# Performance work log

Hardware: AMD Instinct MI355X
Metric: run time of the kernel (lower is better)

## Reference

```python
import jax, jax.numpy as jnp
import numpy as np

DIM = 512
H = 8
D = 64
EPS = 1e-5


def _ln(x, g, b):
    m = jnp.mean(x, axis=-1, keepdims=True)
    v = jnp.var(x, axis=-1, keepdims=True)
    return (x - m) * jax.lax.rsqrt(v + EPS) * g + b


def _attn(x, ctx, wq, wk, wv, wo, bo):
    B, S, _ = x.shape
    T = ctx.shape[1]
    q = (x @ wq).reshape(B, S, H, D)
    k = (ctx @ wk).reshape(B, T, H, D)
    v = (ctx @ wv).reshape(B, T, H, D)
    scale = D ** -0.5
    score = jnp.einsum('bqhd,bkhd->bhqk', q, k) * scale  # [B,H,S,T]
    w = jax.nn.softmax(score, axis=-1)
    o = jnp.einsum('bhqk,bkhd->bqhd', w, v).reshape(B, S, H * D)
    return o @ wo + bo


def _geglu(x, w, b):
    h = x @ w + b
    y, gate = h[..., :4 * DIM], h[..., 4 * DIM:]
    tanh_res = jnp.tanh(gate * 0.7978845608 * (1.0 + 0.044715 * gate * gate))
    return y * 0.5 * gate * (1.0 + tanh_res)


def setup_inputs() -> dict:
    key = jax.random.key(0)
    ks = jax.random.split(key, 16)
    s = 0.02
    inp = {
        'x': jax.random.normal(ks[0], (2, 4096, DIM), jnp.float32),
        'context': jax.random.normal(ks[1], (2, 77, DIM), jnp.float32),
        'ln1_g': jnp.ones((DIM,), jnp.float32),
        'ln1_b': jnp.zeros((DIM,), jnp.float32),
        'wq1': jax.random.normal(ks[2], (DIM, H * D), jnp.float32) * s,
        'wk1': jax.random.normal(ks[3], (DIM, H * D), jnp.float32) * s,
        'wv1': jax.random.normal(ks[4], (DIM, H * D), jnp.float32) * s,
        'wo1': jax.random.normal(ks[5], (H * D, H * D), jnp.float32) * s,
        'bo1': jnp.zeros((H * D,), jnp.float32),
        'ln2_g': jnp.ones((DIM,), jnp.float32),
        'ln2_b': jnp.zeros((DIM,), jnp.float32),
        'wq2': jax.random.normal(ks[6], (DIM, H * D), jnp.float32) * s,
        'wk2': jax.random.normal(ks[7], (DIM, H * D), jnp.float32) * s,
        'wv2': jax.random.normal(ks[8], (DIM, H * D), jnp.float32) * s,
        'wo2': jax.random.normal(ks[9], (H * D, H * D), jnp.float32) * s,
        'bo2': jnp.zeros((H * D,), jnp.float32),
        'ln3_g': jnp.ones((DIM,), jnp.float32),
        'ln3_b': jnp.zeros((DIM,), jnp.float32),
        'geglu_w': jax.random.normal(ks[10], (DIM, 8 * DIM), jnp.float32) * s,
        'geglu_b': jnp.zeros((8 * DIM,), jnp.float32),
        'out_w': jax.random.normal(ks[11], (4 * DIM, DIM), jnp.float32) * s,
        'out_b': jnp.zeros((DIM,), jnp.float32),
    }
    return inp


def reference(x, context, ln1_g, ln1_b, wq1, wk1, wv1, wo1, bo1,
              ln2_g, ln2_b, wq2, wk2, wv2, wo2, bo2,
              ln3_g, ln3_b, geglu_w, geglu_b, out_w, out_b):
    h = _attn(_ln(x, ln1_g, ln1_b), _ln(x, ln1_g, ln1_b), wq1, wk1, wv1, wo1, bo1) + x
    h = _attn(_ln(h, ln2_g, ln2_b), context, wq2, wk2, wv2, wo2, bo2) + h
    ff = _geglu(_ln(h, ln3_g, ln3_b), geglu_w, geglu_b)
    return ff @ out_w + out_b + h
```

## Files before the change

kernel.cpp:

```cpp
#include <hip/hip_runtime.h>
#include <hip/hip_bf16.h>
#include <math.h>

#define DIM 512
#define NHEAD 8
#define HD 64
#define BATCH 2
#define SEQ 4096
#define CTXLEN 77
#define NTOK (BATCH*SEQ)
#define NCTX (BATCH*CTXLEN)

typedef __hip_bfloat16 bf16;
typedef __attribute__((ext_vector_type(8))) short bf8_t;
typedef __attribute__((ext_vector_type(4))) float f4_t;

__device__ __forceinline__ float b2f(bf16 v){ return __bfloat162float(v); }
__device__ __forceinline__ bf16  f2b(float v){ return __float2bfloat16(v); }
__device__ __forceinline__ unsigned int packbf2(float a, float b){
    unsigned int au = __float_as_uint(a) + 0x8000u;
    unsigned int bu = __float_as_uint(b) + 0x8000u;
    return __builtin_amdgcn_perm(bu, au, 0x07060302u);
}
__device__ __forceinline__ void  stf(float* p, float v){ *p = v; }
__device__ __forceinline__ void  stf(bf16* p, float v){ *p = f2b(v); }

__device__ __forceinline__ void glds16(const bf16* g, unsigned short* l){
    __builtin_amdgcn_global_load_lds(
        (__attribute__((address_space(1))) void*)g,
        (__attribute__((address_space(3))) void*)l,
        16, 0, 0);
}

__global__ __launch_bounds__(256)
void ln_kernel(const float* __restrict__ x, const float* __restrict__ g,
               const float* __restrict__ b, bf16* __restrict__ out, int nrows)
{
    int row  = blockIdx.x * 4 + (threadIdx.x >> 6);
    int lane = threadIdx.x & 63;
    if (row >= nrows) return;
    const float* xr = x + (size_t)row * DIM;
    float v[8];
    float s = 0.f, sq = 0.f;
    #pragma unroll
    for (int j = 0; j < 8; ++j) {
        float f = xr[lane + 64*j];
        v[j] = f; s += f; sq += f*f;
    }
    #pragma unroll
    for (int off = 32; off; off >>= 1) {
        s  += __shfl_xor(s,  off);
        sq += __shfl_xor(sq, off);
    }
    float mean = s * (1.f/DIM);
    float var  = sq * (1.f/DIM) - mean*mean;
    float rstd = rsqrtf(var + 1e-5f);
    bf16* orow = out + (size_t)row * DIM;
    #pragma unroll
    for (int j = 0; j < 8; ++j) {
        int c = lane + 64*j;
        orow[c] = f2b((v[j]-mean)*rstd*g[c] + b[c]);
    }
}

__global__ __launch_bounds__(256)
void transpose_bf16_kernel(const float* __restrict__ W, bf16* __restrict__ Wt, int K, int N)
{
    __shared__ float tile[32][33];
    int n0 = blockIdx.x * 32, k0 = blockIdx.y * 32;
    int tx = threadIdx.x & 31, ty = threadIdx.x >> 5;
    #pragma unroll
    for (int p = 0; p < 4; ++p)
        tile[ty + p*8][tx] = W[(size_t)(k0 + ty + p*8)*N + n0 + tx];
    __syncthreads();
    #pragma unroll
    for (int p = 0; p < 4; ++p)
        Wt[(size_t)(n0 + ty + p*8)*K + k0 + tx] = f2b(tile[tx][ty + p*8]);
}

struct TPtrs { const float* src[8]; bf16* dst[8]; };
__global__ __launch_bounds__(256)
void transpose8_kernel(TPtrs p)
{
    __shared__ float tile[32][33];
    const float* W = p.src[blockIdx.z];
    bf16* Wt = p.dst[blockIdx.z];
    int n0 = blockIdx.x * 32, k0 = blockIdx.y * 32;
    int tx = threadIdx.x & 31, ty = threadIdx.x >> 5;
    #pragma unroll
    for (int q = 0; q < 4; ++q)
        tile[ty + q*8][tx] = W[(size_t)(k0 + ty + q*8)*512 + n0 + tx];
    __syncthreads();
    #pragma unroll
    for (int q = 0; q < 4; ++q)
        Wt[(size_t)(n0 + ty + q*8)*512 + k0 + tx] = f2b(tile[tx][ty + q*8]);
}

__global__ __launch_bounds__(256)
void cast_bf16_kernel(const float* __restrict__ in, bf16* __restrict__ out, int n)
{
    int i = blockIdx.x*256 + threadIdx.x;
    if (i < n) out[i] = f2b(in[i]);
}

__global__ __launch_bounds__(256)
void v_transpose_kernel(const bf16* __restrict__ V, bf16* __restrict__ Vt, int T, int pitch)
{
    __shared__ __align__(16) unsigned short tile[64*64];
    const int tid = threadIdx.x;
    const int b = blockIdx.z, h = blockIdx.y;
    const int t0 = blockIdx.x * 64;
    #pragma unroll
    for (int it = 0; it < 2; ++it) {
        int e = tid + it*256;
        int t = e >> 3, c = e & 7;
        int gk = t0 + t;
        bf8_t v = {0,0,0,0,0,0,0,0};
        if (gk < T) v = *(const bf8_t*)(V + ((size_t)(b*T + gk))*DIM + h*HD + c*8);
        *(bf8_t*)&tile[t*64 + c*8] = v;
    }
    __syncthreads();
    #pragma unroll
    for (int it = 0; it < 2; ++it) {
        int e = tid + it*256;
        int d = e & 63, oc = e >> 6;
        unsigned short tmp[8];
        #pragma unroll
        for (int j = 0; j < 8; ++j) tmp[j] = tile[(oc*8 + j)*64 + d];
        *(bf8_t*)(Vt + ((size_t)((b*8 + h)*64 + d))*pitch + t0 + oc*8) = *(bf8_t*)tmp;
    }
}

struct OutPtrs { void* p[3]; };
template<int RESID, typename OUTT, bool GUARD>
__global__ __launch_bounds__(256)
void gemm_mfma_kernel(const bf16* __restrict__ A, const bf16* __restrict__ Wt,
                      const float* __restrict__ bias, const float* __restrict__ resid,
                      OutPtrs outs, int M, int K)
{
    __shared__ __align__(16) unsigned short As[2][128*64];
    __shared__ __align__(16) unsigned short Bs[2][64*64];
    const int tid  = threadIdx.x;
    const int wave = tid >> 6, lane = tid & 63;
    const int l16  = lane & 15, quad = lane >> 4;
    const int wm = (wave >> 1) * 64, wn = (wave & 1) * 32;
    const int m0 = blockIdx.y * 128, n0 = blockIdx.x * 64;
    OUTT* outp = (OUTT*)outs.p[n0 >> 9];
    const int lc0 = n0 & 511;
    const int lr = lane >> 3;
    const int lc = (lane & 7) ^ lr;

    f4_t acc[4][2];
    #pragma unroll
    for (int i = 0; i < 4; ++i) { acc[i][0] = f4_t{0,0,0,0}; acc[i][1] = f4_t{0,0,0,0}; }

    auto stage = [&](int k0, int bf) {
        #pragma unroll
        for (int i = 0; i < 4; ++i) {
            int r = (wave*4 + i)*8 + lr;
            int gr = m0 + r;
            if (GUARD) gr = (gr < M) ? gr : (M-1);
            glds16(A + (size_t)gr*K + k0 + lc*8, &As[bf][(wave*4 + i)*512]);
        }
        #pragma unroll
        for (int j = 0; j < 2; ++j) {
            int r = (wave*2 + j)*8 + lr;
            glds16(Wt + (size_t)(n0 + r)*K + k0 + lc*8, &Bs[bf][(wave*2 + j)*512]);
        }
    };

    stage(0, 0);
    __syncthreads();

    for (int k0 = 0; k0 < K; k0 += 64) {
        const int bf = (k0 >> 6) & 1;
        if (k0 + 64 < K) stage(k0 + 64, bf ^ 1);
        #pragma unroll
        for (int kc = 0; kc < 2; ++kc) {
            const int cg = kc*4 + quad;
            bf8_t af[4], bfr[2];
            #pragma unroll
            for (int mt = 0; mt < 4; ++mt) {
                int r = wm + mt*16 + l16;
                af[mt] = *(const bf8_t*)&As[bf][r*64 + ((cg ^ (r&7))*8)];
            }
            #pragma unroll
            for (int nt = 0; nt < 2; ++nt) {
                int r = wn + nt*16 + l16;
                bfr[nt] = *(const bf8_t*)&Bs[bf][r*64 + ((cg ^ (r&7))*8)];
            }
            #pragma unroll
            for (int mt = 0; mt < 4; ++mt)
                #pragma unroll
                for (int nt = 0; nt < 2; ++nt)
                    acc[mt][nt] = __builtin_amdgcn_mfma_f32_16x16x32_bf16(af[mt], bfr[nt], acc[mt][nt], 0, 0, 0);
        }
        __syncthreads();
    }

    #pragma unroll
    for (int mt = 0; mt < 4; ++mt) {
        #pragma unroll
        for (int r_ = 0; r_ < 4; ++r_) {
            int row = m0 + wm + mt*16 + quad*4 + r_;
            if (GUARD && row >= M) continue;
            size_t rb = (size_t)row * 512;
            #pragma unroll
            for (int nt = 0; nt < 2; ++nt) {
                int col = lc0 + wn + nt*16 + l16;
                float v = acc[mt][nt][r_];
                if (bias) v += bias[col];
                if (RESID) v += resid[rb + col];
                stf(&outp[rb + col], v);
            }
        }
    }
}

__global__ __launch_bounds__(256)
void geglu_mfma_kernel(const bf16* __restrict__ A, const bf16* __restrict__ WtG,
                       const float* __restrict__ bias, bf16* __restrict__ outp)
{
    __shared__ __align__(16) unsigned short As[128*64];
    __shared__ __align__(16) unsigned short Bys[64*64];
    __shared__ __align__(16) unsigned short Bgs[64*64];
    const int tid  = threadIdx.x;
    const int wave = tid >> 6, lane = tid & 63;
    const int l16  = lane & 15, quad = lane >> 4;
    const int m0 = blockIdx.y * 128, n0 = blockIdx.x * 64;
    const int lr = lane >> 3;
    const int lc = (lane & 7) ^ lr;

    f4_t accy[2][4], accg[2][4];
    #pragma unroll
    for (int i = 0; i < 2; ++i)
        #pragma unroll
        for (int j = 0; j < 4; ++j) { accy[i][j] = f4_t{0,0,0,0}; accg[i][j] = f4_t{0,0,0,0}; }

    for (int k0 = 0; k0 < DIM; k0 += 64) {
        #pragma unroll
        for (int i = 0; i < 4; ++i) {
            int r = (wave*4 + i)*8 + lr;
            glds16(A + (size_t)(m0 + r)*DIM + k0 + lc*8, &As[(wave*4 + i)*512]);
        }
        #pragma unroll
        for (int j = 0; j < 2; ++j) {
            int r = (wave*2 + j)*8 + lr;
            glds16(WtG + (size_t)(n0 + r)*DIM + k0 + lc*8, &Bys[(wave*2 + j)*512]);
            glds16(WtG + (size_t)(2048 + n0 + r)*DIM + k0 + lc*8, &Bgs[(wave*2 + j)*512]);
        }
        __syncthreads();
        #pragma unroll
        for (int kc = 0; kc < 2; ++kc) {
            const int cg = kc*4 + quad;
            bf8_t af[2];
            #pragma unroll
            for (int mt = 0; mt < 2; ++mt) {
                int r = wave*32 + mt*16 + l16;
                af[mt] = *(const bf8_t*)&As[r*64 + ((cg ^ (r&7))*8)];
            }
            #pragma unroll
            for (int nt = 0; nt < 4; ++nt) {
                int r = nt*16 + l16;
                bf8_t by = *(const bf8_t*)&Bys[r*64 + ((cg ^ (r&7))*8)];
                bf8_t bg = *(const bf8_t*)&Bgs[r*64 + ((cg ^ (r&7))*8)];
                #pragma unroll
                for (int mt = 0; mt < 2; ++mt) {
                    accy[mt][nt] = __builtin_amdgcn_mfma_f32_16x16x32_bf16(af[mt], by, accy[mt][nt], 0, 0, 0);
                    accg[mt][nt] = __builtin_amdgcn_mfma_f32_16x16x32_bf16(af[mt], bg, accg[mt][nt], 0, 0, 0);
                }
            }
        }
        __syncthreads();
    }

    #pragma unroll
    for (int mt = 0; mt < 2; ++mt) {
        #pragma unroll
        for (int r_ = 0; r_ < 4; ++r_) {
            int row = m0 + wave*32 + mt*16 + quad*4 + r_;
            size_t rb = (size_t)row * 2048;
            #pragma unroll
            for (int nt = 0; nt < 4; ++nt) {
                int col = n0 + nt*16 + l16;
                float y = accy[mt][nt][r_] + bias[col];
                float g = accg[mt][nt][r_] + bias[2048 + col];
                float t = tanhf(0.7978845608f*g*(1.f + 0.044715f*g*g));
                outp[rb + col] = f2b(y * 0.5f * g * (1.f + t));
            }
        }
    }
}

__global__ __launch_bounds__(512)
void attn_mfma_kernel(const bf16* __restrict__ Qm, const bf16* __restrict__ Km,
                      const bf16* __restrict__ VtG, bf16* __restrict__ Om,
                      int T, int vpitch)
{
    __shared__ __align__(16) unsigned short Ks[2][64*64];
    __shared__ __align__(16) unsigned short Vts[2][64*64];

    const int tid  = threadIdx.x;
    const int wave = tid >> 6, lane = tid & 63;
    const int l16  = lane & 15, quad = lane >> 4;
    const int b = blockIdx.z, h = blockIdx.y;
    const int qblk = blockIdx.x * 128;
    const int lr = lane >> 3;
    const int lc = (lane & 7) ^ lr;
    const int srow = wave*8 + lr;

    bf8_t ones;
    #pragma unroll
    for (int j = 0; j < 8; ++j) ((unsigned short*)&ones)[j] = 0x3F80;

    bf8_t qf[2];
    {
        const bf16* qp = Qm + ((size_t)(b*SEQ + qblk + wave*16 + l16))*DIM + h*HD + quad*8;
        #pragma unroll
        for (int kc = 0; kc < 2; ++kc) {
            bf8_t v = *(const bf8_t*)(qp + kc*32);
            unsigned short* u = (unsigned short*)&v;
            unsigned int* w = (unsigned int*)&v;
            #pragma unroll
            for (int j = 0; j < 4; ++j) {
                float f0 = b2f(*(bf16*)&u[2*j])   * 0.1803368801f;
                float f1 = b2f(*(bf16*)&u[2*j+1]) * 0.1803368801f;
                w[j] = packbf2(f0, f1);
            }
            qf[kc] = v;
        }
    }

    f4_t o[4];
    #pragma unroll
    for (int dt = 0; dt < 4; ++dt) o[dt] = f4_t{0,0,0,0};
    f4_t lacc = {0,0,0,0};

    const bf16* Kbase = Km + (size_t)b*T*DIM + h*HD;
    const bf16* Vbase = VtG + ((size_t)((b*8 + h)*64 + srow))*vpitch;

    {
        int gk = srow; if (gk > T-1) gk = T-1;
        glds16(Kbase + (size_t)gk*DIM + lc*8, &Ks[0][wave*512]);
        glds16(Vbase + lc*8,                  &Vts[0][wave*512]);
    }
    __syncthreads();

    const int ntiles = (T + 63) >> 6;
    for (int t0 = 0; t0 < ntiles; ++t0) {
        const int kb = t0 << 6;
        const int cur = t0 & 1;
        if (t0 + 1 < ntiles) {
            int gk = kb + 64 + srow; if (gk > T-1) gk = T-1;
            glds16(Kbase + (size_t)gk*DIM + lc*8,  &Ks[cur^1][wave*512]);
            glds16(Vbase + kb + 64 + lc*8,         &Vts[cur^1][wave*512]);
        }

        bf8_t kf[4][2], vf[4][2];
        #pragma unroll
        for (int t = 0; t < 4; ++t) {
            int r = t*16 + l16;
            #pragma unroll
            for (int kc = 0; kc < 2; ++kc) {
                int cg = kc*4 + quad;
                kf[t][kc] = *(const bf8_t*)&Ks[cur][r*64 + ((cg ^ (r&7))*8)];
                vf[t][kc] = *(const bf8_t*)&Vts[cur][r*64 + ((cg ^ (r&7))*8)];
            }
        }
        const bool tail = (kb + 64 > T);

        f4_t sc4[4];
        #pragma unroll
        for (int km = 0; km < 4; ++km) {
            f4_t c = {0,0,0,0};
            c = __builtin_amdgcn_mfma_f32_16x16x32_bf16(kf[km][0], qf[0], c, 0, 0, 0);
            c = __builtin_amdgcn_mfma_f32_16x16x32_bf16(kf[km][1], qf[1], c, 0, 0, 0);
            sc4[km] = c;
        }
        if (tail) {
            #pragma unroll
            for (int km = 0; km < 4; ++km)
                #pragma unroll
                for (int r = 0; r < 4; ++r)
                    if (kb + km*16 + quad*4 + r >= T) sc4[km][r] = -1e30f;
        }
        unsigned int pk[4][2];
        #pragma unroll
        for (int km = 0; km < 4; ++km) {
            pk[km][0] = packbf2(exp2f(sc4[km][0]), exp2f(sc4[km][1]));
            pk[km][1] = packbf2(exp2f(sc4[km][2]), exp2f(sc4[km][3]));
        }
        #pragma unroll
        for (int kc = 0; kc < 2; ++kc) {
            auto s0 = __builtin_amdgcn_permlane32_swap(pk[2*kc][0], pk[2*kc+1][0], false, false);
            auto w02 = __builtin_amdgcn_permlane16_swap(s0[0], s0[1], false, false);
            auto s1 = __builtin_amdgcn_permlane32_swap(pk[2*kc][1], pk[2*kc+1][1], false, false);
            auto w13 = __builtin_amdgcn_permlane16_swap(s1[0], s1[1], false, false);
            union { unsigned int u[4]; bf8_t v; } pfu;
            pfu.u[0] = w02[0]; pfu.u[1] = w13[0]; pfu.u[2] = w02[1]; pfu.u[3] = w13[1];
            bf8_t pf = pfu.v;
            lacc = __builtin_amdgcn_mfma_f32_16x16x32_bf16(ones, pf, lacc, 0, 0, 0);
            #pragma unroll
            for (int dt = 0; dt < 4; ++dt)
                o[dt] = __builtin_amdgcn_mfma_f32_16x16x32_bf16(vf[dt][kc], pf, o[dt], 0, 0, 0);
        }
        __syncthreads();
    }

    {
        float inv = 1.f / lacc[0];
        int tok = qblk + wave*16 + l16;
        size_t base = ((size_t)(b*SEQ + tok))*DIM + h*HD;
        #pragma unroll
        for (int dt = 0; dt < 4; ++dt) {
            uint2 w;
            w.x = packbf2(o[dt][0]*inv, o[dt][1]*inv);
            w.y = packbf2(o[dt][2]*inv, o[dt][3]*inv);
            *(uint2*)(Om + base + dt*16 + quad*4) = w;
        }
    }
}

extern "C" void kernel_launch(void* const* d_in, const int* in_sizes, int n_in,
                              void* d_out, int out_size, void* d_ws, size_t ws_size,
                              hipStream_t stream)
{
    (void)in_sizes; (void)n_in; (void)out_size; (void)ws_size;
    const float* x    = (const float*)d_in[0];
    const float* ctx  = (const float*)d_in[1];
    const float* ln1g = (const float*)d_in[2];
    const float* ln1b = (const float*)d_in[3];
    const float* wq1  = (const float*)d_in[4];
    const float* wk1  = (const float*)d_in[5];
    const float* wv1  = (const float*)d_in[6];
    const float* wo1  = (const float*)d_in[7];
    const float* bo1  = (const float*)d_in[8];
    const float* ln2g = (const float*)d_in[9];
    const float* ln2b = (const float*)d_in[10];
    const float* wq2  = (const float*)d_in[11];
    const float* wk2  = (const float*)d_in[12];
    const float* wv2  = (const float*)d_in[13];
    const float* wo2  = (const float*)d_in[14];
    const float* bo2  = (const float*)d_in[15];
    const float* ln3g = (const float*)d_in[16];
    const float* ln3b = (const float*)d_in[17];
    const float* gw   = (const float*)d_in[18];
    const float* gb   = (const float*)d_in[19];
    const float* ow   = (const float*)d_in[20];
    const float* ob   = (const float*)d_in[21];
    float* out = (float*)d_out;

    char* ws = (char*)d_ws;
    bf16* An  = (bf16*)(ws);
    bf16* VtG = (bf16*)(ws);
    bf16* Qb  = (bf16*)(ws + ((size_t)8<<20));
    bf16* Kb  = (bf16*)(ws + ((size_t)16<<20));
    bf16* Vb  = (bf16*)(ws + ((size_t)24<<20));
    bf16* Ob  = (bf16*)(ws + ((size_t)32<<20));
    bf16* FF  = Qb;
    float* Hf = out;
    bf16* WT  = (bf16*)(ws + ((size_t)40<<20));
    bf16* wq1T = WT + 0*262144, *wk1T = WT + 1*262144, *wv1T = WT + 2*262144, *wo1T = WT + 3*262144;
    bf16* wq2T = WT + 4*262144, *wk2T = WT + 5*262144, *wv2T = WT + 6*262144, *wo2T = WT + 7*262144;
    bf16* gwT  = (bf16*)(ws + ((size_t)44<<20));
    bf16* owT  = (bf16*)(ws + ((size_t)48<<20));
    bf16* ctxb = (bf16*)(ws + ((size_t)50<<20));
    bf16* VtG2 = (bf16*)(ws + ((size_t)50<<20) + ((size_t)512<<10));

    dim3 blk(256);
    dim3 blkA(512);

    TPtrs tp;
    tp.src[0]=wq1; tp.src[1]=wk1; tp.src[2]=wv1; tp.src[3]=wo1;
    tp.src[4]=wq2; tp.src[5]=wk2; tp.src[6]=wv2; tp.src[7]=wo2;
    tp.dst[0]=wq1T; tp.dst[1]=wk1T; tp.dst[2]=wv1T; tp.dst[3]=wo1T;
    tp.dst[4]=wq2T; tp.dst[5]=wk2T; tp.dst[6]=wv2T; tp.dst[7]=wo2T;
    transpose8_kernel<<<dim3(16,16,8), blk, 0, stream>>>(tp);
    transpose_bf16_kernel<<<dim3(128,16), blk, 0, stream>>>(gw, gwT, DIM, 4096);
    transpose_bf16_kernel<<<dim3(16,64), blk, 0, stream>>>(ow, owT, 2048, DIM);
    cast_bf16_kernel<<<dim3((NCTX*DIM+255)/256), blk, 0, stream>>>(ctx, ctxb, NCTX*DIM);

    dim3 gLN(NTOK/4);
    dim3 gQKV(24, 64);
    dim3 gG(8, 64);
    dim3 gKVx(16, 2);
    dim3 gGEGLU(32, 64);
    dim3 gATT(SEQ/128, NHEAD, BATCH);
    OutPtrs oQKV{{Qb, Kb, Vb}};
    OutPtrs oKVx{{Kb, Vb, nullptr}};
    OutPtrs oQ{{Qb, nullptr, nullptr}};
    OutPtrs oH{{Hf, nullptr, nullptr}};
    OutPtrs oOut{{out, nullptr, nullptr}};

    ln_kernel<<<gLN, blk, 0, stream>>>(x, ln1g, ln1b, An, NTOK);
    gemm_mfma_kernel<0,bf16,false><<<gQKV, blk, 0, stream>>>(An, wq1T, nullptr, nullptr, oQKV, NTOK, DIM);
    v_transpose_kernel<<<dim3(SEQ/64, NHEAD, BATCH), blk, 0, stream>>>(Vb, VtG, SEQ, SEQ);
    attn_mfma_kernel<<<gATT, blkA, 0, stream>>>(Qb, Kb, VtG, Ob, SEQ, SEQ);
    gemm_mfma_kernel<1,float,false><<<gG, blk, 0, stream>>>(Ob, wo1T, bo1, x, oH, NTOK, DIM);

    ln_kernel<<<gLN, blk, 0, stream>>>(Hf, ln2g, ln2b, An, NTOK);
    gemm_mfma_kernel<0,bf16,false><<<gG, blk, 0, stream>>>(An, wq2T, nullptr, nullptr, oQ, NTOK, DIM);
    gemm_mfma_kernel<0,bf16,true><<<gKVx, blk, 0, stream>>>(ctxb, wk2T, nullptr, nullptr, oKVx, NCTX, DIM);
    v_transpose_kernel<<<dim3(2, NHEAD, BATCH), blk, 0, stream>>>(Vb, VtG2, CTXLEN, 128);
    attn_mfma_kernel<<<gATT, blkA, 0, stream>>>(Qb, Kb, VtG2, Ob, CTXLEN, 128);
    gemm_mfma_kernel<1,float,false><<<gG, blk, 0, stream>>>(Ob, wo2T, bo2, Hf, oH, NTOK, DIM);

    ln_kernel<<<gLN, blk, 0, stream>>>(Hf, ln3g, ln3b, An, NTOK);
    geglu_mfma_kernel<<<gGEGLU, blk, 0, stream>>>(An, gwT, gb, FF);
    gemm_mfma_kernel<1,float,false><<<gG, blk, 0, stream>>>(FF, owT, ob, Hf, oOut, NTOK, 2048);
}
```

Before: 472.2 us.

## Add 128x128 GEMM tile kernel and restage attention K/V and P through LDS

Adds a 128x128-tile MFMA GEMM and uses it for the fused QKV projection and the FFN output projection. Larger tiles raise operand reuse but halve the block count, leaving only 256 blocks for the output GEMM. Separately, the attention kernel drops the double-buffered direct-to-LDS K/V loads for register-staged single-buffer stores with an extra barrier per tile. It also replaces the permlane swaps that reshuffle P with a write and read through a per-wave LDS scratch. This trades cross-lane permutes for extra LDS traffic and loses overlap between loads and compute.

```diff
diff --git a/kernel.cpp b/kernel.cpp
--- a/kernel.cpp
+++ b/kernel.cpp
@@ -132,6 +132,7 @@
 }
 
 struct OutPtrs { void* p[3]; };
+
 template<int RESID, typename OUTT, bool GUARD>
 __global__ __launch_bounds__(256)
 void gemm_mfma_kernel(const bf16* __restrict__ A, const bf16* __restrict__ Wt,
@@ -217,6 +218,93 @@
     }
 }
 
+template<int RESID, typename OUTT, bool GUARD>
+__global__ __launch_bounds__(256)
+void gemm128_kernel(const bf16* __restrict__ A, const bf16* __restrict__ Wt,
+                    const float* __restrict__ bias, const float* __restrict__ resid,
+                    OutPtrs outs, int M, int K)
+{
+    __shared__ __align__(16) unsigned short As[2][128*64];
+    __shared__ __align__(16) unsigned short Bs[2][128*64];
+    const int tid  = threadIdx.x;
+    const int wave = tid >> 6, lane = tid & 63;
+    const int l16  = lane & 15, quad = lane >> 4;
+    const int wm = (wave >> 1) * 64, wn = (wave & 1) * 64;
+    const int m0 = blockIdx.y * 128, n0 = blockIdx.x * 128;
+    OUTT* outp = (OUTT*)outs.p[n0 >> 9];
+    const int lc0 = n0 & 511;
+    const int lr = lane >> 3;
+    const int lc = (lane & 7) ^ lr;
+
+    f4_t acc[4][4];
+    #pragma unroll
+    for (int i = 0; i < 4; ++i)
+        #pragma unroll
+        for (int j = 0; j < 4; ++j) acc[i][j] = f4_t{0,0,0,0};
+
+    auto stage = [&](int k0, int bf) {
+        #pragma unroll
+        for (int i = 0; i < 4; ++i) {
+            int r = (wave*4 + i)*8 + lr;
+            int gr = m0 + r;
+            if (GUARD) gr = (gr < M) ? gr : (M-1);
+            glds16(A + (size_t)gr*K + k0 + lc*8, &As[bf][(wave*4 + i)*512]);
+        }
+        #pragma unroll
+        for (int i = 0; i < 4; ++i) {
+            int r = (wave*4 + i)*8 + lr;
+            glds16(Wt + (size_t)(n0 + r)*K + k0 + lc*8, &Bs[bf][(wave*4 + i)*512]);
+        }
+    };
+
+    stage(0, 0);
+    __syncthreads();
+
+    for (int k0 = 0; k0 < K; k0 += 64) {
+        const int bf = (k0 >> 6) & 1;
+        if (k0 + 64 < K) stage(k0 + 64, bf ^ 1);
+        #pragma unroll
+        for (int kc = 0; kc < 2; ++kc) {
+            const int cg = kc*4 + quad;
+            bf8_t af[4], bfr[4];
+            #pragma unroll
+            for (int mt = 0; mt < 4; ++mt) {
+                int r = wm + mt*16 + l16;
+                af[mt] = *(const bf8_t*)&As[bf][r*64 + ((cg ^ (r&7))*8)];
+            }
+            #pragma unroll
+            for (int nt = 0; nt < 4; ++nt) {
+                int r = wn + nt*16 + l16;
+                bfr[nt] = *(const bf8_t*)&Bs[bf][r*64 + ((cg ^ (r&7))*8)];
+            }
+            #pragma unroll
+            for (int mt = 0; mt < 4; ++mt)
+                #pragma unroll
+                for (int nt = 0; nt < 4; ++nt)
+                    acc[mt][nt] = __builtin_amdgcn_mfma_f32_16x16x32_bf16(af[mt], bfr[nt], acc[mt][nt], 0, 0, 0);
+        }
+        __syncthreads();
+    }
+
+    #pragma unroll
+    for (int mt = 0; mt < 4; ++mt) {
+        #pragma unroll
+        for (int r_ = 0; r_ < 4; ++r_) {
+            int row = m0 + wm + mt*16 + quad*4 + r_;
+            if (GUARD && row >= M) continue;
+            size_t rb = (size_t)row * 512;
+            #pragma unroll
+            for (int nt = 0; nt < 4; ++nt) {
+                int col = lc0 + wn + nt*16 + l16;
+                float v = acc[mt][nt][r_];
+                if (bias) v += bias[col];
+                if (RESID) v += resid[rb + col];
+                stf(&outp[rb + col], v);
+            }
+        }
+    }
+}
+
 __global__ __launch_bounds__(256)
 void geglu_mfma_kernel(const bf16* __restrict__ A, const bf16* __restrict__ WtG,
                        const float* __restrict__ bias, bf16* __restrict__ outp)
@@ -297,17 +385,16 @@
                       const bf16* __restrict__ VtG, bf16* __restrict__ Om,
                       int T, int vpitch)
 {
-    __shared__ __align__(16) unsigned short Ks[2][64*64];
-    __shared__ __align__(16) unsigned short Vts[2][64*64];
+    __shared__ __align__(16) unsigned short Ks[64*64];
+    __shared__ __align__(16) unsigned short Vts[64*64];
+    __shared__ __align__(16) unsigned short Ps[8][16*64];
 
     const int tid  = threadIdx.x;
     const int wave = tid >> 6, lane = tid & 63;
     const int l16  = lane & 15, quad = lane >> 4;
     const int b = blockIdx.z, h = blockIdx.y;
     const int qblk = blockIdx.x * 128;
-    const int lr = lane >> 3;
-    const int lc = (lane & 7) ^ lr;
-    const int srow = wave*8 + lr;
+    const int sr = tid >> 3, sc_ = tid & 7;
 
     bf8_t ones;
     #pragma unroll
@@ -337,23 +424,24 @@
     f4_t lacc = {0,0,0,0};
 
     const bf16* Kbase = Km + (size_t)b*T*DIM + h*HD;
-    const bf16* Vbase = VtG + ((size_t)((b*8 + h)*64 + srow))*vpitch;
-
-    {
-        int gk = srow; if (gk > T-1) gk = T-1;
-        glds16(Kbase + (size_t)gk*DIM + lc*8, &Ks[0][wave*512]);
-        glds16(Vbase + lc*8,                  &Vts[0][wave*512]);
-    }
-    __syncthreads();
+    const bf16* Vbase = VtG + ((size_t)((b*8 + h)*64 + sr))*vpitch;
+
+    bf8_t kq, vq;
+    kq = bf8_t{0,0,0,0,0,0,0,0};
+    if (sr < T) kq = *(const bf8_t*)(Kbase + (size_t)sr*DIM + sc_*8);
+    vq = *(const bf8_t*)(Vbase + sc_*8);
 
     const int ntiles = (T + 63) >> 6;
     for (int t0 = 0; t0 < ntiles; ++t0) {
         const int kb = t0 << 6;
-        const int cur = t0 & 1;
+        *(bf8_t*)&Ks[sr*64 + ((sc_ ^ (sr&7))*8)]  = kq;
+        *(bf8_t*)&Vts[sr*64 + ((sc_ ^ (sr&7))*8)] = vq;
+        __syncthreads();
         if (t0 + 1 < ntiles) {
-            int gk = kb + 64 + srow; if (gk > T-1) gk = T-1;
-            glds16(Kbase + (size_t)gk*DIM + lc*8,  &Ks[cur^1][wave*512]);
-            glds16(Vbase + kb + 64 + lc*8,         &Vts[cur^1][wave*512]);
+            int gk = kb + 64 + sr;
+            kq = bf8_t{0,0,0,0,0,0,0,0};
+            if (gk < T) kq = *(const bf8_t*)(Kbase + (size_t)gk*DIM + sc_*8);
+            vq = *(const bf8_t*)(Vbase + kb + 64 + sc_*8);
         }
 
         bf8_t kf[4][2], vf[4][2];
@@ -363,8 +451,8 @@
             #pragma unroll
             for (int kc = 0; kc < 2; ++kc) {
                 int cg = kc*4 + quad;
-                kf[t][kc] = *(const bf8_t*)&Ks[cur][r*64 + ((cg ^ (r&7))*8)];
-                vf[t][kc] = *(const bf8_t*)&Vts[cur][r*64 + ((cg ^ (r&7))*8)];
+                kf[t][kc] = *(const bf8_t*)&Ks[r*64 + ((cg ^ (r&7))*8)];
+                vf[t][kc] = *(const bf8_t*)&Vts[r*64 + ((cg ^ (r&7))*8)];
             }
         }
         const bool tail = (kb + 64 > T);
@@ -384,21 +472,19 @@
                 for (int r = 0; r < 4; ++r)
                     if (kb + km*16 + quad*4 + r >= T) sc4[km][r] = -1e30f;
         }
-        unsigned int pk[4][2];
         #pragma unroll
         for (int km = 0; km < 4; ++km) {
-            pk[km][0] = packbf2(exp2f(sc4[km][0]), exp2f(sc4[km][1]));
-            pk[km][1] = packbf2(exp2f(sc4[km][2]), exp2f(sc4[km][3]));
+            uint2 w;
+            w.x = packbf2(exp2f(sc4[km][0]), exp2f(sc4[km][1]));
+            w.y = packbf2(exp2f(sc4[km][2]), exp2f(sc4[km][3]));
+            int chunk = 2*km + (quad >> 1);
+            int a = l16*64 + ((chunk ^ (l16 & 7))*8) + (quad & 1)*4;
+            *(uint2*)&Ps[wave][a] = w;
         }
         #pragma unroll
         for (int kc = 0; kc < 2; ++kc) {
-            auto s0 = __builtin_amdgcn_permlane32_swap(pk[2*kc][0], pk[2*kc+1][0], false, false);
-            auto w02 = __builtin_amdgcn_permlane16_swap(s0[0], s0[1], false, false);
-            auto s1 = __builtin_amdgcn_permlane32_swap(pk[2*kc][1], pk[2*kc+1][1], false, false);
-            auto w13 = __builtin_amdgcn_permlane16_swap(s1[0], s1[1], false, false);
-            union { unsigned int u[4]; bf8_t v; } pfu;
-            pfu.u[0] = w02[0]; pfu.u[1] = w13[0]; pfu.u[2] = w02[1]; pfu.u[3] = w13[1];
-            bf8_t pf = pfu.v;
+            int cg = kc*4 + quad;
+            bf8_t pf = *(const bf8_t*)&Ps[wave][l16*64 + ((cg ^ (l16 & 7))*8)];
             lacc = __builtin_amdgcn_mfma_f32_16x16x32_bf16(ones, pf, lacc, 0, 0, 0);
             #pragma unroll
             for (int dt = 0; dt < 4; ++dt)
@@ -481,10 +567,11 @@
     cast_bf16_kernel<<<dim3((NCTX*DIM+255)/256), blk, 0, stream>>>(ctx, ctxb, NCTX*DIM);
 
     dim3 gLN(NTOK/4);
-    dim3 gQKV(24, 64);
+    dim3 gQKV(12, 64);
     dim3 gG(8, 64);
     dim3 gKVx(16, 2);
     dim3 gGEGLU(32, 64);
+    dim3 gOUT(4, 64);
     dim3 gATT(SEQ/128, NHEAD, BATCH);
     OutPtrs oQKV{{Qb, Kb, Vb}};
     OutPtrs oKVx{{Kb, Vb, nullptr}};
@@ -493,7 +580,7 @@
     OutPtrs oOut{{out, nullptr, nullptr}};
 
     ln_kernel<<<gLN, blk, 0, stream>>>(x, ln1g, ln1b, An, NTOK);
-    gemm_mfma_kernel<0,bf16,false><<<gQKV, blk, 0, stream>>>(An, wq1T, nullptr, nullptr, oQKV, NTOK, DIM);
+    gemm128_kernel<0,bf16,false><<<gQKV, blk, 0, stream>>>(An, wq1T, nullptr, nullptr, oQKV, NTOK, DIM);
     v_transpose_kernel<<<dim3(SEQ/64, NHEAD, BATCH), blk, 0, stream>>>(Vb, VtG, SEQ, SEQ);
     attn_mfma_kernel<<<gATT, blkA, 0, stream>>>(Qb, Kb, VtG, Ob, SEQ, SEQ);
     gemm_mfma_kernel<1,float,false><<<gG, blk, 0, stream>>>(Ob, wo1T, bo1, x, oH, NTOK, DIM);
@@ -507,5 +594,5 @@
 
     ln_kernel<<<gLN, blk, 0, stream>>>(Hf, ln3g, ln3b, An, NTOK);
     geglu_mfma_kernel<<<gGEGLU, blk, 0, stream>>>(An, gwT, gb, FF);
-    gemm_mfma_kernel<1,float,false><<<gG, blk, 0, stream>>>(FF, owT, ob, Hf, oOut, NTOK, 2048);
-}
+    gemm128_kernel<1,float,false><<<gOUT, blk, 0, stream>>>(FF, owT, ob, Hf, oOut, NTOK, 2048);
+}
```

New measurement: 480.1 us. No clear change (+1.7%).
